# Kernel optimization log

Hardware: AMD Instinct MI355X
Metric: run time of the kernel (lower is better)

## Reference

```python
import jax, jax.numpy as jnp
import numpy as np

EPS = 1e-06
SR = 22050
HOP = 512
INIT_T = 0.06


def setup_inputs() -> dict:
    key = jax.random.key(0)
    mel_spec = jax.random.uniform(key, (32, 128, 8192), dtype=jnp.float32)  # nonneg mel power
    alpha = jnp.float32(0.98)
    delta = jnp.float32(2.0)
    r = jnp.float32(0.5)
    s = jnp.float32(HOP / (SR * INIT_T))  # fixed smoothing coefficient (buffer)
    return {"mel_spec": mel_spec, "alpha": alpha, "delta": delta, "r": r, "s": s}


def _pcen_iir(mel_spec, s):
    # EMA along last (time) axis: M[t] = (1-s)*M[t-1] + s*x[t], M[0] = x[0]
    x = jnp.moveaxis(mel_spec, -1, 0)  # [T, B, F]

    def step(m, xt):
        m = (1.0 - s) * m + s * xt
        return m, m

    _, Ms = jax.lax.scan(step, x[0], x[1:])
    M = jnp.concatenate([x[:1], Ms], axis=0)
    return jnp.moveaxis(M, 0, -1)  # [B, F, T]


def reference(mel_spec, alpha, delta, r, s):
    alpha_c = jnp.clip(alpha, 0.01, 0.99)
    delta_c = jnp.abs(delta) + EPS
    r_c = jnp.clip(r, 0.01, 1.0)
    M = _pcen_iir(mel_spec, s)
    smooth = jnp.power(EPS + M, alpha_c)
    pcen = jnp.power(mel_spec / (smooth + 1e-06) + delta_c, r_c) - jnp.power(delta_c, r_c)
    return pcen
```

## Files before the change

kernel.cpp:

```cpp
#include <hip/hip_runtime.h>
#include <math.h>


#define T_LEN 8192
#define TILE  256
#define HALF  4096
#define NT    16

typedef float v4f __attribute__((ext_vector_type(4)));

__device__ __forceinline__ float fexp2(float x){ return __builtin_amdgcn_exp2f(x); }
__device__ __forceinline__ float flog2(float x){ return __builtin_amdgcn_logf(x); }
__device__ __forceinline__ float frcp (float x){ return __builtin_amdgcn_rcpf(x); }
__device__ __forceinline__ float readlane_f(float v, int l) {
    return __builtin_bit_cast(float, __builtin_amdgcn_readlane(__builtin_bit_cast(int, v), l));
}
__device__ __forceinline__ float readfirst_f(float v) {
    return __builtin_bit_cast(float, __builtin_amdgcn_readfirstlane(__builtin_bit_cast(int, v)));
}

__global__ __launch_bounds__(256) void pcen_kernel(
    const float* __restrict__ x,
    const float* __restrict__ p_alpha, const float* __restrict__ p_delta,
    const float* __restrict__ p_r,     const float* __restrict__ p_s,
    float* __restrict__ out)
{
    const int tid  = threadIdx.x;
    const int wave = tid >> 6;
    const int lane = tid & 63;
    const int row  = blockIdx.x * 2 + (wave >> 1);
    const int half = wave & 1;
    const long long rbase = (long long)row * T_LEN;
    const float* rp = x + rbase + half * HALF + lane * 4;
    float*       op = out + rbase + half * HALF + lane * 4;

    const float alpha_c = fminf(fmaxf(p_alpha[0], 0.01f), 0.99f);
    const float delta_c = fabsf(p_delta[0]) + 1e-6f;
    const float r_c     = fminf(fmaxf(p_r[0], 0.01f), 1.0f);
    const float s       = p_s[0];
    const float om      = 1.0f - s;
    const bool  rhalf   = (r_c == 0.5f);
    const float dr      = rhalf ? __builtin_sqrtf(delta_c)
                                : fexp2(r_c * flog2(delta_c));

    const float wDl = s, wCl = s*om, wBl = wCl*om, wAl = wBl*om;
    const float om2 = om*om, om4 = om2*om2;

    float pw = 1.0f, b = om4;
    #pragma unroll
    for (int k = 0; k < 6; ++k) {
        if ((lane >> k) & 1) pw *= b;
        b *= b;
    }
    const float om256 = b;

    const int t_first = half ? -1 : 0;

    float4 cur = *reinterpret_cast<const float4*>(rp + (long long)t_first * TILE);
    int t1 = t_first + 1; if (t1 > NT - 1) t1 = NT - 1;
    float4 nxt = *reinterpret_cast<const float4*>(rp + (long long)t1 * TILE);

    float carry = half ? 0.0f : readfirst_f(cur.x);

    for (int t = t_first; t < NT; ++t) {
        float4 v = cur;
        cur = nxt;
        int tn = t + 2; if (tn > NT - 1) tn = NT - 1;
        nxt = *reinterpret_cast<const float4*>(rp + (long long)tn * TILE);

        float d = fmaf(wAl, v.x, fmaf(wBl, v.y, fmaf(wCl, v.z, wDl * v.w)));

        float m0 = d, w = om4;
        #pragma unroll
        for (int k = 0; k < 6; ++k) {
            float up = __shfl_up(m0, 1u << k, 64);
            if (lane >= (1 << k)) m0 = fmaf(w, up, m0);
            w = w * w;
        }

        float m0prev = __shfl_up(m0, 1, 64);
        float base_p = (lane == 0) ? 0.0f : m0prev;
        float Mstart = fmaf(pw, carry, base_p);

        float m63 = readlane_f(m0, 63);
        carry = fmaf(om256, carry, m63);

        if (t >= 0) {
            float M0 = fmaf(om, Mstart, s * v.x);
            float M1 = fmaf(om, M0,     s * v.y);
            float M2 = fmaf(om, M1,     s * v.z);
            float M3 = fmaf(om, M2,     s * v.w);

            float s0 = fexp2(alpha_c * flog2(1e-6f + M0));
            float s1 = fexp2(alpha_c * flog2(1e-6f + M1));
            float s2 = fexp2(alpha_c * flog2(1e-6f + M2));
            float s3 = fexp2(alpha_c * flog2(1e-6f + M3));
            float b0 = fmaf(v.x, frcp(s0 + 1e-6f), delta_c);
            float b1 = fmaf(v.y, frcp(s1 + 1e-6f), delta_c);
            float b2 = fmaf(v.z, frcp(s2 + 1e-6f), delta_c);
            float b3 = fmaf(v.w, frcp(s3 + 1e-6f), delta_c);

            v4f o;
            if (rhalf) {
                o.x = __builtin_sqrtf(b0) - dr;
                o.y = __builtin_sqrtf(b1) - dr;
                o.z = __builtin_sqrtf(b2) - dr;
                o.w = __builtin_sqrtf(b3) - dr;
            } else {
                o.x = fexp2(r_c * flog2(b0)) - dr;
                o.y = fexp2(r_c * flog2(b1)) - dr;
                o.z = fexp2(r_c * flog2(b2)) - dr;
                o.w = fexp2(r_c * flog2(b3)) - dr;
            }
            __builtin_nontemporal_store(
                o, reinterpret_cast<v4f*>(op + (long long)t * TILE));
        }
    }
}

extern "C" void kernel_launch(void* const* d_in, const int* in_sizes, int n_in,
                              void* d_out, int out_size, void* d_ws, size_t ws_size,
                              hipStream_t stream) {
    const float* x     = (const float*)d_in[0];
    const float* alpha = (const float*)d_in[1];
    const float* delta = (const float*)d_in[2];
    const float* r     = (const float*)d_in[3];
    const float* s     = (const float*)d_in[4];
    float* out = (float*)d_out;

    const int rows = in_sizes[0] / T_LEN;
    const int grid = rows / 2;
    pcen_kernel<<<grid, 256, 0, stream>>>(x, alpha, delta, r, s, out);
}
```

Before: 50.13 us.

## Process eight contiguous elements per lane to halve wave scans per row

Each lane now handles 8 contiguous time samples (two float4 loads) instead of 4, so a tile covers 512 samples and each half-row needs 8 tiles instead of 16. This halves the number of shuffle-based wave scans and carry updates per row and doubles the independent work per iteration. Loads become 32-byte strided per lane, which may coalesce less cleanly, and the per-lane serial recurrence grows longer. Stores also switch from nontemporal to regular stores.

```diff
diff --git a/kernel.cpp b/kernel.cpp
--- a/kernel.cpp
+++ b/kernel.cpp
@@ -3,9 +3,9 @@
 
 
 #define T_LEN 8192
-#define TILE  256
 #define HALF  4096
-#define NT    16
+#define NT    8
+#define TV    128
 
 typedef float v4f __attribute__((ext_vector_type(4)));
 
@@ -31,8 +31,8 @@
     const int row  = blockIdx.x * 2 + (wave >> 1);
     const int half = wave & 1;
     const long long rbase = (long long)row * T_LEN;
-    const float* rp = x + rbase + half * HALF + lane * 4;
-    float*       op = out + rbase + half * HALF + lane * 4;
+    const float* rp = x + rbase + half * HALF + lane * 8;
+    float*       op = out + rbase + half * HALF + lane * 8;
 
     const float alpha_c = fminf(fmaxf(p_alpha[0], 0.01f), 0.99f);
     const float delta_c = fabsf(p_delta[0]) + 1e-6f;
@@ -44,33 +44,39 @@
                                 : fexp2(r_c * flog2(delta_c));
 
     const float wDl = s, wCl = s*om, wBl = wCl*om, wAl = wBl*om;
-    const float om2 = om*om, om4 = om2*om2;
+    const float om2 = om*om, om4 = om2*om2, om8 = om4*om4;
 
-    float pw = 1.0f, b = om4;
+    float pw = 1.0f, b = om8;
     #pragma unroll
     for (int k = 0; k < 6; ++k) {
         if ((lane >> k) & 1) pw *= b;
         b *= b;
     }
-    const float om256 = b;
+    const float om512 = b;
 
     const int t_first = half ? -1 : 0;
 
-    float4 cur = *reinterpret_cast<const float4*>(rp + (long long)t_first * TILE);
+    const v4f* rpv = reinterpret_cast<const v4f*>(rp);
+    v4f curA = rpv[(long long)t_first * TV];
+    v4f curB = rpv[(long long)t_first * TV + 1];
     int t1 = t_first + 1; if (t1 > NT - 1) t1 = NT - 1;
-    float4 nxt = *reinterpret_cast<const float4*>(rp + (long long)t1 * TILE);
+    v4f nxtA = rpv[(long long)t1 * TV];
+    v4f nxtB = rpv[(long long)t1 * TV + 1];
 
-    float carry = half ? 0.0f : readfirst_f(cur.x);
+    float carry = half ? 0.0f : readfirst_f(curA.x);
 
     for (int t = t_first; t < NT; ++t) {
-        float4 v = cur;
-        cur = nxt;
+        v4f a = curA, c = curB;
+        curA = nxtA; curB = nxtB;
         int tn = t + 2; if (tn > NT - 1) tn = NT - 1;
-        nxt = *reinterpret_cast<const float4*>(rp + (long long)tn * TILE);
+        nxtA = rpv[(long long)tn * TV];
+        nxtB = rpv[(long long)tn * TV + 1];
 
-        float d = fmaf(wAl, v.x, fmaf(wBl, v.y, fmaf(wCl, v.z, wDl * v.w)));
+        float c0 = fmaf(wAl, a.x, fmaf(wBl, a.y, fmaf(wCl, a.z, wDl * a.w)));
+        float c1 = fmaf(wAl, c.x, fmaf(wBl, c.y, fmaf(wCl, c.z, wDl * c.w)));
+        float d  = fmaf(c0, om4, c1);
 
-        float m0 = d, w = om4;
+        float m0 = d, w = om8;
         #pragma unroll
         for (int k = 0; k < 6; ++k) {
             float up = __shfl_up(m0, 1u << k, 64);
@@ -83,37 +89,58 @@
         float Mstart = fmaf(pw, carry, base_p);
 
         float m63 = readlane_f(m0, 63);
-        carry = fmaf(om256, carry, m63);
+        carry = fmaf(om512, carry, m63);
 
         if (t >= 0) {
-            float M0 = fmaf(om, Mstart, s * v.x);
-            float M1 = fmaf(om, M0,     s * v.y);
-            float M2 = fmaf(om, M1,     s * v.z);
-            float M3 = fmaf(om, M2,     s * v.w);
+            float M0 = fmaf(om, Mstart, s * a.x);
+            float M1 = fmaf(om, M0,     s * a.y);
+            float M2 = fmaf(om, M1,     s * a.z);
+            float M3 = fmaf(om, M2,     s * a.w);
+            float M4 = fmaf(om, M3,     s * c.x);
+            float M5 = fmaf(om, M4,     s * c.y);
+            float M6 = fmaf(om, M5,     s * c.z);
+            float M7 = fmaf(om, M6,     s * c.w);
 
             float s0 = fexp2(alpha_c * flog2(1e-6f + M0));
             float s1 = fexp2(alpha_c * flog2(1e-6f + M1));
             float s2 = fexp2(alpha_c * flog2(1e-6f + M2));
             float s3 = fexp2(alpha_c * flog2(1e-6f + M3));
-            float b0 = fmaf(v.x, frcp(s0 + 1e-6f), delta_c);
-            float b1 = fmaf(v.y, frcp(s1 + 1e-6f), delta_c);
-            float b2 = fmaf(v.z, frcp(s2 + 1e-6f), delta_c);
-            float b3 = fmaf(v.w, frcp(s3 + 1e-6f), delta_c);
+            float s4 = fexp2(alpha_c * flog2(1e-6f + M4));
+            float s5 = fexp2(alpha_c * flog2(1e-6f + M5));
+            float s6 = fexp2(alpha_c * flog2(1e-6f + M6));
+            float s7 = fexp2(alpha_c * flog2(1e-6f + M7));
+            float b0 = fmaf(a.x, frcp(s0 + 1e-6f), delta_c);
+            float b1 = fmaf(a.y, frcp(s1 + 1e-6f), delta_c);
+            float b2 = fmaf(a.z, frcp(s2 + 1e-6f), delta_c);
+            float b3 = fmaf(a.w, frcp(s3 + 1e-6f), delta_c);
+            float b4 = fmaf(c.x, frcp(s4 + 1e-6f), delta_c);
+            float b5 = fmaf(c.y, frcp(s5 + 1e-6f), delta_c);
+            float b6 = fmaf(c.z, frcp(s6 + 1e-6f), delta_c);
+            float b7 = fmaf(c.w, frcp(s7 + 1e-6f), delta_c);
 
-            v4f o;
+            v4f oA, oB;
             if (rhalf) {
-                o.x = __builtin_sqrtf(b0) - dr;
-                o.y = __builtin_sqrtf(b1) - dr;
-                o.z = __builtin_sqrtf(b2) - dr;
-                o.w = __builtin_sqrtf(b3) - dr;
+                oA.x = __builtin_sqrtf(b0) - dr;
+                oA.y = __builtin_sqrtf(b1) - dr;
+                oA.z = __builtin_sqrtf(b2) - dr;
+                oA.w = __builtin_sqrtf(b3) - dr;
+                oB.x = __builtin_sqrtf(b4) - dr;
+                oB.y = __builtin_sqrtf(b5) - dr;
+                oB.z = __builtin_sqrtf(b6) - dr;
+                oB.w = __builtin_sqrtf(b7) - dr;
             } else {
-                o.x = fexp2(r_c * flog2(b0)) - dr;
-                o.y = fexp2(r_c * flog2(b1)) - dr;
-                o.z = fexp2(r_c * flog2(b2)) - dr;
-                o.w = fexp2(r_c * flog2(b3)) - dr;
+                oA.x = fexp2(r_c * flog2(b0)) - dr;
+                oA.y = fexp2(r_c * flog2(b1)) - dr;
+                oA.z = fexp2(r_c * flog2(b2)) - dr;
+                oA.w = fexp2(r_c * flog2(b3)) - dr;
+                oB.x = fexp2(r_c * flog2(b4)) - dr;
+                oB.y = fexp2(r_c * flog2(b5)) - dr;
+                oB.z = fexp2(r_c * flog2(b6)) - dr;
+                oB.w = fexp2(r_c * flog2(b7)) - dr;
             }
-            __builtin_nontemporal_store(
-                o, reinterpret_cast<v4f*>(op + (long long)t * TILE));
+            v4f* opv = reinterpret_cast<v4f*>(op);
+            opv[(long long)t * TV]     = oA;
+            opv[(long long)t * TV + 1] = oB;
         }
     }
 }
```

Result: slower. 52.55 us (+4.8%).
